# Kernel optimization log

Measured on AMD Instinct MI355X. Metric: run time of the kernel, lower is better.

Reference implementation:

```python
import jax, jax.numpy as jnp
import numpy as np

B, S, D, H = 4, 1024, 1024, 16
HD = D // H  # 64, even for RoPE


def _rope_tables(seq_len, head_dim):
    inv_freq = 1.0 / (10000.0 ** (jnp.arange(0, head_dim, 2, dtype=jnp.float32) / head_dim))
    pos = jnp.arange(seq_len, dtype=jnp.float32)
    ang = pos[:, None] * inv_freq[None, :]           # [S, HD/2]
    return jnp.cos(ang), jnp.sin(ang)


def _apply_rope(x, cos, sin):
    # x: [B, S, H, HD]; cos/sin: [S, HD/2] broadcast to [1, S, 1, HD/2]
    c = cos[None, :, None, :]
    s = sin[None, :, None, :]
    x1 = x[..., 0::2]
    x2 = x[..., 1::2]
    return jnp.concatenate([x1 * c - x2 * s, x1 * s + x2 * c], axis=-1)


def setup_inputs() -> dict:
    key = jax.random.key(0)
    ks = jax.random.split(key, 11)
    sc = 1.0 / np.sqrt(D)
    inp = {
        "query": jax.random.normal(ks[0], (B, S, D), jnp.float32),
        "key": jax.random.normal(ks[1], (B, S, D), jnp.float32),
        "value": jax.random.normal(ks[2], (B, S, D), jnp.float32),
        "mask": jnp.tril(jnp.ones((S, S), jnp.int32))[None, None],  # causal [1,1,S,S]
        "Wq": jax.random.normal(ks[3], (D, D), jnp.float32) * sc,
        "bq": jnp.zeros((D,), jnp.float32),
        "Wk": jax.random.normal(ks[4], (D, D), jnp.float32) * sc,
        "bk": jnp.zeros((D,), jnp.float32),
        "Wv": jax.random.normal(ks[5], (D, D), jnp.float32) * sc,
        "bv": jnp.zeros((D,), jnp.float32),
        "Wo": jax.random.normal(ks[6], (D, D), jnp.float32) * sc,
        "bo": jnp.zeros((D,), jnp.float32),
    }
    return inp


def reference(query, key, value, mask, Wq, bq, Wk, bk, Wv, bv, Wo, bo):
    Bq, Sq, _ = query.shape
    Sk = key.shape[1]
    q = (query @ Wq + bq).reshape(Bq, Sq, H, HD)
    k = (key @ Wk + bk).reshape(Bq, Sk, H, HD)
    v = (value @ Wv + bv).reshape(Bq, Sk, H, HD)
    cos, sin = _rope_tables(max(Sq, Sk), HD)
    q = _apply_rope(q, cos[:Sq], sin[:Sq])
    k = _apply_rope(k, cos[:Sk], sin[:Sk])
    scores = jnp.einsum("bqhd,bkhd->bhqk", q, k) / jnp.sqrt(jnp.float32(HD))
    scores = jnp.where(mask == 0, jnp.float32(-jnp.inf), scores)
    attn = jax.nn.softmax(scores, axis=-1)  # dropout p=0 (inference)
    ctx = jnp.einsum("bhqk,bkhd->bqhd", attn, v).reshape(Bq, Sq, D)
    return ctx @ Wo + bo
```

## Files before the change

kernel.cpp:

```cpp
#include <hip/hip_runtime.h>
#include <hip/hip_bf16.h>
#include <math.h>

#define B_DIM 4
#define S_DIM 1024
#define D_DIM 1024
#define H_DIM 16
#define HD_DIM 64
#define M_TOT 4096

typedef short short8 __attribute__((ext_vector_type(8)));
typedef float f32x4 __attribute__((ext_vector_type(4)));

__device__ inline float bf2f(short u)
{
    return __uint_as_float(((unsigned)(unsigned short)u) << 16);
}

__device__ inline void gload_lds16(const void* gsrc, void* lds)
{
    __builtin_amdgcn_global_load_lds(
        (const __attribute__((address_space(1))) unsigned int*)gsrc,
        (__attribute__((address_space(3))) unsigned int*)lds, 16, 0, 0);
}

__global__ __launch_bounds__(256) void preamble_kernel(
    const float* __restrict__ W0, const float* __restrict__ W1,
    const float* __restrict__ W2, const float* __restrict__ W3,
    __hip_bfloat16* __restrict__ T0, __hip_bfloat16* __restrict__ T1,
    __hip_bfloat16* __restrict__ T2, __hip_bfloat16* __restrict__ T3,
    float* __restrict__ tab)
{
    const int tid = threadIdx.x;
    if (blockIdx.z == 4) {
        const int fb = blockIdx.y * 32 + blockIdx.x;
        if (fb >= 128) return;
        const int t = fb * 256 + tid;
        const int pos = t >> 5, i = t & 31;
        float inv = powf(10000.0f, -(float)(2 * i) / 64.0f);
        float ang = (float)pos * inv;
        float s, c;
        sincosf(ang, &s, &c);
        tab[t] = c;
        tab[32768 + t] = s;
        return;
    }

    const float* W = (blockIdx.z == 0) ? W0 : (blockIdx.z == 1) ? W1
                    : (blockIdx.z == 2) ? W2 : W3;
    __hip_bfloat16* T = (blockIdx.z == 0) ? T0 : (blockIdx.z == 1) ? T1
                       : (blockIdx.z == 2) ? T2 : T3;

    __shared__ float tile[32][33];
    const int r = tid >> 3;
    const int c4 = (tid & 7) * 4;

    float4 v = *(const float4*)&W[(long)(blockIdx.y * 32 + r) * D_DIM + blockIdx.x * 32 + c4];
    tile[r][c4 + 0] = v.x;
    tile[r][c4 + 1] = v.y;
    tile[r][c4 + 2] = v.z;
    tile[r][c4 + 3] = v.w;
    __syncthreads();

    __hip_bfloat16 o[4];
    o[0] = __float2bfloat16(tile[c4 + 0][r]);
    o[1] = __float2bfloat16(tile[c4 + 1][r]);
    o[2] = __float2bfloat16(tile[c4 + 2][r]);
    o[3] = __float2bfloat16(tile[c4 + 3][r]);
    *(uint2*)&T[(long)(blockIdx.x * 32 + r) * D_DIM + blockIdx.y * 32 + c4] = *(uint2*)o;
}

__global__ __launch_bounds__(256, 3) void gemm_qkv_kernel(
    const float* __restrict__ Xq, const float* __restrict__ Xk,
    const float* __restrict__ Xv,
    const __hip_bfloat16* __restrict__ WtQ, const __hip_bfloat16* __restrict__ WtK,
    const __hip_bfloat16* __restrict__ WtV,
    const float* __restrict__ bq, const float* __restrict__ bk,
    const float* __restrict__ bv,
    __hip_bfloat16* __restrict__ Qo, __hip_bfloat16* __restrict__ Ko,
    __hip_bfloat16* __restrict__ Vto)
{
    __shared__ __align__(16) __hip_bfloat16 Al[2][128][40];
    __shared__ __align__(16) __hip_bfloat16 Bl[2][128][32];

    const int F = blockIdx.x + 8 * blockIdx.y + 256 * blockIdx.z;
    const int xcd = F & 7;
    const int sb = F >> 3;
    const int z = sb >> 5;
    const int n0 = (sb & 7) * 128;
    const int m0 = ((xcd << 2) | ((sb >> 3) & 3)) * 128;

    const float* X = (z == 0) ? Xq : (z == 1) ? Xk : Xv;
    const __hip_bfloat16* Wt = (z == 0) ? WtQ : (z == 1) ? WtK : WtV;
    const float* bias = (z == 0) ? bq : (z == 1) ? bk : bv;

    const int tid = threadIdx.x;
    const int l = tid & 63;
    const int w = tid >> 6;

    const int srow = w * 16 + (l >> 2);
    const int skc = (l & 3) * 8;
    const __hip_bfloat16* Bbase = Wt + (long)(n0 + srow) * D_DIM + skc;
    char* ldsB0 = (char*)&Bl[0][0][0] + w * 1024;
    char* ldsB1 = (char*)&Bl[1][0][0] + w * 1024;

    const int arow = tid >> 1;
    const int ak = (tid & 1) * 16;
    const float* Af = X + (long)(m0 + arow) * D_DIM + ak;

    const int lrow = l & 15;
    const int kg = l >> 4;
    const int wr = (w >> 1) * 64;
    const int wc = (w & 1) * 64;

    f32x4 acc[4][4];
#pragma unroll
    for (int i = 0; i < 4; ++i)
#pragma unroll
        for (int j = 0; j < 4; ++j) acc[i][j] = (f32x4){0.f, 0.f, 0.f, 0.f};

    float4 f0, f1, f2, f3;

    {
        f0 = *(const float4*)(Af);
        f1 = *(const float4*)(Af + 4);
        f2 = *(const float4*)(Af + 8);
        f3 = *(const float4*)(Af + 12);
        float fa[16] = {f0.x, f0.y, f0.z, f0.w, f1.x, f1.y, f1.z, f1.w,
                        f2.x, f2.y, f2.z, f2.w, f3.x, f3.y, f3.z, f3.w};
        __attribute__((aligned(16))) __hip_bfloat16 ab[16];
#pragma unroll
        for (int i = 0; i < 16; ++i) ab[i] = __float2bfloat16(fa[i]);
        *(short8*)&Al[0][arow][ak]     = ((const short8*)ab)[0];
        *(short8*)&Al[0][arow][ak + 8] = ((const short8*)ab)[1];
        gload_lds16(Bbase, ldsB0);
        gload_lds16(Bbase + 64 * D_DIM, ldsB0 + 4096);
        asm volatile("" ::: "memory");
        f0 = *(const float4*)(Af + 32);
        f1 = *(const float4*)(Af + 36);
        f2 = *(const float4*)(Af + 40);
        f3 = *(const float4*)(Af + 44);
        asm volatile("s_waitcnt vmcnt(4)" ::: "memory");
        asm volatile("s_waitcnt lgkmcnt(0)" ::: "memory");
        __builtin_amdgcn_s_barrier();
    }

    for (int t = 0; t < 32; ++t) {
        const int p = t & 1;
        const int q = p ^ 1;
        char* ldsBq = (q == 0) ? ldsB0 : ldsB1;

        if (t < 31) {
            const int k1 = (t + 1) * 32;
            gload_lds16(Bbase + k1, ldsBq);
            gload_lds16(Bbase + 64 * D_DIM + k1, ldsBq + 4096);
            float fa[16] = {f0.x, f0.y, f0.z, f0.w, f1.x, f1.y, f1.z, f1.w,
                            f2.x, f2.y, f2.z, f2.w, f3.x, f3.y, f3.z, f3.w};
            __attribute__((aligned(16))) __hip_bfloat16 ab[16];
#pragma unroll
            for (int i = 0; i < 16; ++i) ab[i] = __float2bfloat16(fa[i]);
            *(short8*)&Al[q][arow][ak]     = ((const short8*)ab)[0];
            *(short8*)&Al[q][arow][ak + 8] = ((const short8*)ab)[1];
        }
        asm volatile("" ::: "memory");
        if (t < 30) {
            const int k2 = (t + 2) * 32;
            f0 = *(const float4*)(Af + k2);
            f1 = *(const float4*)(Af + k2 + 4);
            f2 = *(const float4*)(Af + k2 + 8);
            f3 = *(const float4*)(Af + k2 + 12);
        }

        short8 af[4], bf[4];
#pragma unroll
        for (int i = 0; i < 4; ++i)
            af[i] = *(const short8*)&Al[p][wr + i * 16 + lrow][kg * 8];
#pragma unroll
        for (int j = 0; j < 4; ++j)
            bf[j] = *(const short8*)&Bl[p][wc + j * 16 + lrow][kg * 8];
#pragma unroll
        for (int i = 0; i < 4; ++i)
#pragma unroll
            for (int j = 0; j < 4; ++j)
                acc[i][j] = __builtin_amdgcn_mfma_f32_16x16x32_bf16(
                    af[i], bf[j], acc[i][j], 0, 0, 0);

        if (t < 31) {
            if (t < 30)
                asm volatile("s_waitcnt vmcnt(4)" ::: "memory");
            else
                asm volatile("s_waitcnt vmcnt(0)" ::: "memory");
            asm volatile("s_waitcnt lgkmcnt(0)" ::: "memory");
            __builtin_amdgcn_s_barrier();
        }
    }

#pragma unroll
    for (int i = 0; i < 4; ++i) {
#pragma unroll
        for (int j = 0; j < 4; ++j) {
            const int col = n0 + wc + j * 16 + lrow;
            const float bvs = bias[col];
            const int rbase = m0 + wr + i * 16 + kg * 4;
            if (z < 2) {
                __hip_bfloat16* Out = (z == 0) ? Qo : Ko;
#pragma unroll
                for (int r = 0; r < 4; ++r)
                    Out[(long)(rbase + r) * D_DIM + col] =
                        __float2bfloat16(acc[i][j][r] + bvs);
            } else {
                const int hh = col >> 6, dd = col & 63;
                const int bb = rbase >> 10, s0 = rbase & 1023;
                __hip_bfloat16 o[4];
#pragma unroll
                for (int r = 0; r < 4; ++r)
                    o[r] = __float2bfloat16(acc[i][j][r] + bvs);
                *(uint2*)&Vto[((long)((bb * H_DIM + hh) * HD_DIM + dd)) * S_DIM + s0] =
                    *(uint2*)o;
            }
        }
    }
}

__global__ __launch_bounds__(256, 2) void gemm_wo_kernel(
    const __hip_bfloat16* __restrict__ X, const __hip_bfloat16* __restrict__ Wt,
    const float* __restrict__ bias, float* __restrict__ Out)
{
    __shared__ __align__(16) __hip_bfloat16 Al[128][32];
    __shared__ __align__(16) __hip_bfloat16 Bl[64][32];

    const int F = blockIdx.x;
    const int xcd = F & 7;
    const int s = F >> 3;
    const int n0 = (s & 15) * 64;
    const int m0 = ((xcd << 2) | (s >> 4)) * 128;

    const int tid = threadIdx.x;
    const int l = tid & 63;
    const int w = tid >> 6;

    const int srow = w * 16 + (l >> 2);
    const int skc = (l & 3) * 8;
    const __hip_bfloat16* Abase = X + (long)(m0 + srow) * D_DIM + skc;
    const __hip_bfloat16* Bbase = Wt + (long)(n0 + srow) * D_DIM + skc;
    char* ldsA0 = (char*)&Al[0][0] + w * 1024;
    char* ldsB0 = (char*)&Bl[0][0] + w * 1024;

    const int lrow = l & 15;
    const int kg = l >> 4;
    const int wr = (w >> 1) * 64;
    const int wc = (w & 1) * 32;

    f32x4 acc[4][2];
#pragma unroll
    for (int i = 0; i < 4; ++i)
#pragma unroll
        for (int j = 0; j < 2; ++j) acc[i][j] = (f32x4){0.f, 0.f, 0.f, 0.f};

    for (int k0 = 0; k0 < D_DIM; k0 += 32) {
        __syncthreads();
        gload_lds16(Abase + k0, ldsA0);
        gload_lds16(Abase + 64 * D_DIM + k0, ldsA0 + 4096);
        gload_lds16(Bbase + k0, ldsB0);
        __syncthreads();

        short8 af[4], bf[2];
#pragma unroll
        for (int i = 0; i < 4; ++i)
            af[i] = *(const short8*)&Al[wr + i * 16 + lrow][kg * 8];
#pragma unroll
        for (int j = 0; j < 2; ++j)
            bf[j] = *(const short8*)&Bl[wc + j * 16 + lrow][kg * 8];
#pragma unroll
        for (int i = 0; i < 4; ++i)
#pragma unroll
            for (int j = 0; j < 2; ++j)
                acc[i][j] = __builtin_amdgcn_mfma_f32_16x16x32_bf16(
                    af[i], bf[j], acc[i][j], 0, 0, 0);
    }

#pragma unroll
    for (int i = 0; i < 4; ++i) {
#pragma unroll
        for (int j = 0; j < 2; ++j) {
            const int col = n0 + wc + j * 16 + lrow;
            const float bv = bias[col];
            const int rbase = m0 + wr + i * 16 + kg * 4;
#pragma unroll
            for (int r = 0; r < 4; ++r)
                Out[(long)(rbase + r) * D_DIM + col] = acc[i][j][r] + bv;
        }
    }
}

__global__ __launch_bounds__(256) void rope_bf16_kernel(
    const __hip_bfloat16* __restrict__ Qi, const __hip_bfloat16* __restrict__ Ki,
    __hip_bfloat16* __restrict__ Qo, __hip_bfloat16* __restrict__ Ko,
    const float* __restrict__ tab)
{
    const long t = (long)blockIdx.x * 256 + threadIdx.x;
    const int row = (int)(t >> 7);
    const int slot = (int)(t & 127);
    const int hh = slot >> 3;
    const int p0 = (slot & 7) * 4;
    const int pos = row & (S_DIM - 1);
    const bool isQ = (blockIdx.y == 0);
    const float scale = isQ ? 0.125f : 1.0f;

    const __hip_bfloat16* src = (isQ ? Qi : Ki) + (long)row * D_DIM + hh * HD_DIM;
    __hip_bfloat16* dst = (isQ ? Qo : Ko) + (long)row * D_DIM + hh * HD_DIM;

    short8 xv = *(const short8*)&src[2 * p0];
    float4 cv = *(const float4*)&tab[pos * 32 + p0];
    float4 sv = *(const float4*)&tab[32768 + pos * 32 + p0];
    float cc[4] = {cv.x, cv.y, cv.z, cv.w};
    float ss[4] = {sv.x, sv.y, sv.z, sv.w};

    __hip_bfloat16 o1[4], o2[4];
#pragma unroll
    for (int j = 0; j < 4; ++j) {
        float x1 = bf2f(xv[2 * j]);
        float x2 = bf2f(xv[2 * j + 1]);
        o1[j] = __float2bfloat16((x1 * cc[j] - x2 * ss[j]) * scale);
        o2[j] = __float2bfloat16((x1 * ss[j] + x2 * cc[j]) * scale);
    }
    *(uint2*)&dst[p0]      = *(uint2*)o1;
    *(uint2*)&dst[p0 + 32] = *(uint2*)o2;
}

#define KPAD 72

__global__ __launch_bounds__(256, 2) void attn_mfma_kernel(
    const __hip_bfloat16* __restrict__ Q,
    const __hip_bfloat16* __restrict__ K,
    const __hip_bfloat16* __restrict__ Vt,
    __hip_bfloat16* __restrict__ CTX)
{
    __shared__ __align__(16) __hip_bfloat16 Kl[64][KPAD];
    __shared__ __align__(16) __hip_bfloat16 Vl[64][KPAD];
    __shared__ __align__(16) __hip_bfloat16 Pl[4][32][KPAD];
    __shared__ __align__(16) float aS[4][2][16];

    const int tid = threadIdx.x;
    const int l = tid & 63;
    const int w = tid >> 6;

    const int bid = blockIdx.x + 8 * blockIdx.y + 128 * blockIdx.z;
    const int half = bid >> 8;
    const int idx = bid & 255;
    int qt = idx & 7;
    if (half) qt = 7 - qt;
    const int rest = idx >> 3;
    const int h = rest & 15;
    const int b = (rest >> 4) | (half << 1);

    const int lrow = l & 15;
    const int kg = l >> 4;
    const int kg4 = kg * 4;

    const int q0w = qt * 128 + w * 32;
    const long qrow_base = (long)b * S_DIM + q0w;

    short8 qf[2][2];
#pragma unroll
    for (int m = 0; m < 2; ++m)
#pragma unroll
        for (int ks = 0; ks < 2; ++ks)
            qf[m][ks] = *(const short8*)&Q[(qrow_base + m * 16 + lrow) * D_DIM +
                                           h * HD_DIM + ks * 32 + kg * 8];

    f32x4 ctx[2][4];
#pragma unroll
    for (int m = 0; m < 2; ++m)
#pragma unroll
        for (int d = 0; d < 4; ++d) ctx[m][d] = (f32x4){0.f, 0.f, 0.f, 0.f};
    float mrun[2] = {-1e30f, -1e30f};
    float lrun[2] = {0.f, 0.f};

    const int sr = tid >> 2;
    const int sc2 = (tid & 3) * 16;
    const __hip_bfloat16* Kg = K + ((long)b * S_DIM + sr) * D_DIM + h * HD_DIM + sc2;
    const __hip_bfloat16* Vg = Vt + ((long)((b * H_DIM + h) * HD_DIM) + sr) * S_DIM + sc2;

    const int ktmax = 2 * qt + 1;

    short8 kp0 = *(const short8*)Kg;
    short8 kp1 = *(const short8*)(Kg + 8);
    short8 vp0 = *(const short8*)Vg;
    short8 vp1 = *(const short8*)(Vg + 8);

    for (int kt = 0; kt <= ktmax; ++kt) {
        __syncthreads();
        *(short8*)&Kl[sr][sc2]     = kp0;
        *(short8*)&Kl[sr][sc2 + 8] = kp1;
        *(short8*)&Vl[sr][sc2]     = vp0;
        *(short8*)&Vl[sr][sc2 + 8] = vp1;
        if (kt < ktmax) {
            const __hip_bfloat16* kp = Kg + (long)(kt + 1) * 64 * D_DIM;
            const __hip_bfloat16* vp = Vg + (kt + 1) * 64;
            kp0 = *(const short8*)kp;
            kp1 = *(const short8*)(kp + 8);
            vp0 = *(const short8*)vp;
            vp1 = *(const short8*)(vp + 8);
        }
        __syncthreads();

        if (kt * 64 > q0w + 31) continue;

        f32x4 sac[2][4];
#pragma unroll
        for (int m = 0; m < 2; ++m)
#pragma unroll
            for (int nt = 0; nt < 4; ++nt) sac[m][nt] = (f32x4){0.f, 0.f, 0.f, 0.f};

        short8 kf[4][2];
#pragma unroll
        for (int nt = 0; nt < 4; ++nt)
#pragma unroll
            for (int ks = 0; ks < 2; ++ks)
                kf[nt][ks] = *(const short8*)&Kl[nt * 16 + lrow][ks * 32 + kg * 8];
#pragma unroll
        for (int m = 0; m < 2; ++m)
#pragma unroll
            for (int nt = 0; nt < 4; ++nt)
#pragma unroll
                for (int ks = 0; ks < 2; ++ks)
                    sac[m][nt] = __builtin_amdgcn_mfma_f32_16x16x32_bf16(
                        kf[nt][ks], qf[m][ks], sac[m][nt], 0, 0, 0);

        const bool partial = (kt * 64 + 63 > q0w);
        const int kbase = kt * 64;
#pragma unroll
        for (int m = 0; m < 2; ++m) {
            const int qg = q0w + m * 16 + lrow;
            float s[16];
#pragma unroll
            for (int nt = 0; nt < 4; ++nt)
#pragma unroll
                for (int r = 0; r < 4; ++r) {
                    float v = sac[m][nt][r];
                    if (partial && (kbase + nt * 16 + kg4 + r > qg)) v = -1e30f;
                    s[nt * 4 + r] = v;
                }
            float t8[8];
#pragma unroll
            for (int i = 0; i < 8; ++i) t8[i] = fmaxf(s[i], s[i + 8]);
#pragma unroll
            for (int i = 0; i < 4; ++i) t8[i] = fmaxf(t8[i], t8[i + 4]);
            float mx = fmaxf(fmaxf(t8[0], t8[1]), fmaxf(t8[2], t8[3]));
            mx = fmaxf(mx, __shfl_xor(mx, 16));
            mx = fmaxf(mx, __shfl_xor(mx, 32));
            const float mnew = fmaxf(mrun[m], mx);
            const float alpha = __expf(mrun[m] - mnew);
            mrun[m] = mnew;

            float p0s = 0.f, p1s = 0.f, p2s = 0.f, p3s = 0.f;
            __attribute__((aligned(8))) __hip_bfloat16 pb[16];
#pragma unroll
            for (int i = 0; i < 4; ++i) {
                float p = __expf(s[i] - mnew);      p0s += p; pb[i] = __float2bfloat16(p);
            }
#pragma unroll
            for (int i = 4; i < 8; ++i) {
                float p = __expf(s[i] - mnew);      p1s += p; pb[i] = __float2bfloat16(p);
            }
#pragma unroll
            for (int i = 8; i < 12; ++i) {
                float p = __expf(s[i] - mnew);      p2s += p; pb[i] = __float2bfloat16(p);
            }
#pragma unroll
            for (int i = 12; i < 16; ++i) {
                float p = __expf(s[i] - mnew);      p3s += p; pb[i] = __float2bfloat16(p);
            }
            float sum = (p0s + p1s) + (p2s + p3s);
            sum += __shfl_xor(sum, 16);
            sum += __shfl_xor(sum, 32);
            lrun[m] = lrun[m] * alpha + sum;

            if (kg == 0) aS[w][m][lrow] = alpha;
#pragma unroll
            for (int nt = 0; nt < 4; ++nt)
                *(uint2*)&Pl[w][m * 16 + lrow][nt * 16 + kg4] = *(uint2*)&pb[nt * 4];
        }

#pragma unroll
        for (int m = 0; m < 2; ++m) {
            f32x4 al4 = *(const f32x4*)&aS[w][m][kg4];
#pragma unroll
            for (int dt = 0; dt < 4; ++dt)
#pragma unroll
                for (int r = 0; r < 4; ++r) ctx[m][dt][r] *= al4[r];
        }

        short8 vf[4][2];
#pragma unroll
        for (int dt = 0; dt < 4; ++dt)
#pragma unroll
            for (int ks = 0; ks < 2; ++ks)
                vf[dt][ks] = *(const short8*)&Vl[dt * 16 + lrow][ks * 32 + kg * 8];
#pragma unroll
        for (int m = 0; m < 2; ++m) {
            short8 pf[2];
#pragma unroll
            for (int ks = 0; ks < 2; ++ks)
                pf[ks] = *(const short8*)&Pl[w][m * 16 + lrow][ks * 32 + kg * 8];
#pragma unroll
            for (int dt = 0; dt < 4; ++dt)
#pragma unroll
                for (int ks = 0; ks < 2; ++ks)
                    ctx[m][dt] = __builtin_amdgcn_mfma_f32_16x16x32_bf16(
                        pf[ks], vf[dt][ks], ctx[m][dt], 0, 0, 0);
        }
    }

    if (kg == 0) {
        aS[w][0][lrow] = lrun[0];
        aS[w][1][lrow] = lrun[1];
    }
#pragma unroll
    for (int m = 0; m < 2; ++m) {
        f32x4 lv = *(const f32x4*)&aS[w][m][kg4];
#pragma unroll
        for (int r = 0; r < 4; ++r) {
            const float inv_l = 1.0f / lv[r];
            const long rowoff = (qrow_base + m * 16 + kg4 + r) * D_DIM + h * HD_DIM;
#pragma unroll
            for (int dt = 0; dt < 4; ++dt)
                CTX[rowoff + dt * 16 + lrow] = __float2bfloat16(ctx[m][dt][r] * inv_l);
        }
    }
}

extern "C" void kernel_launch(void* const* d_in, const int* in_sizes, int n_in,
                              void* d_out, int out_size, void* d_ws, size_t ws_size,
                              hipStream_t stream)
{
    const float* query = (const float*)d_in[0];
    const float* key   = (const float*)d_in[1];
    const float* value = (const float*)d_in[2];
    const float* Wq = (const float*)d_in[4];
    const float* bq = (const float*)d_in[5];
    const float* Wk = (const float*)d_in[6];
    const float* bk = (const float*)d_in[7];
    const float* Wv = (const float*)d_in[8];
    const float* bv = (const float*)d_in[9];
    const float* Wo = (const float*)d_in[10];
    const float* bo = (const float*)d_in[11];

    char* wsb = (char*)d_ws;
    __hip_bfloat16* Qw    = (__hip_bfloat16*)(wsb);
    __hip_bfloat16* Kw    = (__hip_bfloat16*)(wsb + (8L  << 20));
    __hip_bfloat16* Vtb   = (__hip_bfloat16*)(wsb + (16L << 20));
    __hip_bfloat16* Qr    = (__hip_bfloat16*)(wsb + (24L << 20));
    __hip_bfloat16* Kr    = (__hip_bfloat16*)(wsb + (32L << 20));
    __hip_bfloat16* CTXbf = (__hip_bfloat16*)(wsb + (40L << 20));
    __hip_bfloat16* WtQ   = (__hip_bfloat16*)(wsb + (48L << 20));
    __hip_bfloat16* WtK   = (__hip_bfloat16*)(wsb + (50L << 20));
    __hip_bfloat16* WtV   = (__hip_bfloat16*)(wsb + (52L << 20));
    __hip_bfloat16* WtO   = (__hip_bfloat16*)(wsb + (54L << 20));
    float*          tab   = (float*)(wsb + (56L << 20));

    preamble_kernel<<<dim3(32, 32, 5), 256, 0, stream>>>(
        Wq, Wk, Wv, Wo, WtQ, WtK, WtV, WtO, tab);

    gemm_qkv_kernel<<<dim3(8, 32, 3), 256, 0, stream>>>(
        query, key, value, WtQ, WtK, WtV, bq, bk, bv, Qw, Kw, Vtb);

    rope_bf16_kernel<<<dim3(2048, 2), 256, 0, stream>>>(Qw, Kw, Qr, Kr, tab);

    attn_mfma_kernel<<<dim3(8, 16, 4), 256, 0, stream>>>(Qr, Kr, Vtb, CTXbf);

    gemm_wo_kernel<<<512, 256, 0, stream>>>(CTXbf, WtO, bo, (float*)d_out);
}
```

Before: 110.9 us.

## Triple-buffer weight tiles in QKV GEMM with prefetch distance two

The QKV projection GEMM moves from a double-buffered to a triple-buffered LDS ring for the weight (B) tiles, issuing async global-to-LDS loads two K-steps ahead. The K loop is manually unrolled by two, with a second register set for the fp32 activation prefetch, and the explicit vmcnt waits are dropped in favour of the compiler's waits on those registers. A sched_barrier places the fp32-to-bf16 conversion and LDS store of the next A tile after the MFMA block, aiming to hide global latency and overlap conversion with matrix math. The change costs 8 KB more LDS per block and more registers, which could reduce occupancy under the 3-blocks-per-CU launch bound. Correctness of the B tiles relies on in-order vmcnt retirement rather than explicit waits.

```diff
diff --git a/kernel.cpp b/kernel.cpp
--- a/kernel.cpp
+++ b/kernel.cpp
@@ -81,7 +81,7 @@
     __hip_bfloat16* __restrict__ Vto)
 {
     __shared__ __align__(16) __hip_bfloat16 Al[2][128][40];
-    __shared__ __align__(16) __hip_bfloat16 Bl[2][128][32];
+    __shared__ __align__(16) __hip_bfloat16 Bl[3][128][32];
 
     const int F = blockIdx.x + 8 * blockIdx.y + 256 * blockIdx.z;
     const int xcd = F & 7;
@@ -101,8 +101,7 @@
     const int srow = w * 16 + (l >> 2);
     const int skc = (l & 3) * 8;
     const __hip_bfloat16* Bbase = Wt + (long)(n0 + srow) * D_DIM + skc;
-    char* ldsB0 = (char*)&Bl[0][0][0] + w * 1024;
-    char* ldsB1 = (char*)&Bl[1][0][0] + w * 1024;
+    char* ldsBw = (char*)&Bl[0][0][0] + w * 1024;
 
     const int arow = tid >> 1;
     const int ak = (tid & 1) * 16;
@@ -120,6 +119,7 @@
         for (int j = 0; j < 4; ++j) acc[i][j] = (f32x4){0.f, 0.f, 0.f, 0.f};
 
     float4 f0, f1, f2, f3;
+    float4 g0, g1, g2, g3;
 
     {
         f0 = *(const float4*)(Af);
@@ -133,65 +133,108 @@
         for (int i = 0; i < 16; ++i) ab[i] = __float2bfloat16(fa[i]);
         *(short8*)&Al[0][arow][ak]     = ((const short8*)ab)[0];
         *(short8*)&Al[0][arow][ak + 8] = ((const short8*)ab)[1];
-        gload_lds16(Bbase, ldsB0);
-        gload_lds16(Bbase + 64 * D_DIM, ldsB0 + 4096);
+        gload_lds16(Bbase, ldsBw);
+        gload_lds16(Bbase + 64 * D_DIM, ldsBw + 4096);
+        gload_lds16(Bbase + 32, ldsBw + 8192);
+        gload_lds16(Bbase + 64 * D_DIM + 32, ldsBw + 8192 + 4096);
         asm volatile("" ::: "memory");
         f0 = *(const float4*)(Af + 32);
         f1 = *(const float4*)(Af + 36);
         f2 = *(const float4*)(Af + 40);
         f3 = *(const float4*)(Af + 44);
-        asm volatile("s_waitcnt vmcnt(4)" ::: "memory");
+        asm volatile("s_waitcnt vmcnt(6)" ::: "memory");
         asm volatile("s_waitcnt lgkmcnt(0)" ::: "memory");
         __builtin_amdgcn_s_barrier();
     }
 
-    for (int t = 0; t < 32; ++t) {
-        const int p = t & 1;
-        const int q = p ^ 1;
-        char* ldsBq = (q == 0) ? ldsB0 : ldsB1;
-
-        if (t < 31) {
-            const int k1 = (t + 1) * 32;
-            gload_lds16(Bbase + k1, ldsBq);
-            gload_lds16(Bbase + 64 * D_DIM + k1, ldsBq + 4096);
-            float fa[16] = {f0.x, f0.y, f0.z, f0.w, f1.x, f1.y, f1.z, f1.w,
-                            f2.x, f2.y, f2.z, f2.w, f3.x, f3.y, f3.z, f3.w};
-            __attribute__((aligned(16))) __hip_bfloat16 ab[16];
-#pragma unroll
-            for (int i = 0; i < 16; ++i) ab[i] = __float2bfloat16(fa[i]);
-            *(short8*)&Al[q][arow][ak]     = ((const short8*)ab)[0];
-            *(short8*)&Al[q][arow][ak + 8] = ((const short8*)ab)[1];
-        }
-        asm volatile("" ::: "memory");
-        if (t < 30) {
-            const int k2 = (t + 2) * 32;
-            f0 = *(const float4*)(Af + k2);
-            f1 = *(const float4*)(Af + k2 + 4);
-            f2 = *(const float4*)(Af + k2 + 8);
-            f3 = *(const float4*)(Af + k2 + 12);
-        }
-
-        short8 af[4], bf[4];
-#pragma unroll
-        for (int i = 0; i < 4; ++i)
-            af[i] = *(const short8*)&Al[p][wr + i * 16 + lrow][kg * 8];
-#pragma unroll
-        for (int j = 0; j < 4; ++j)
-            bf[j] = *(const short8*)&Bl[p][wc + j * 16 + lrow][kg * 8];
-#pragma unroll
-        for (int i = 0; i < 4; ++i)
+    int bc = 0;
+#pragma unroll 1
+    for (int tt = 0; tt < 16; ++tt) {
+        {
+            const int t = 2 * tt;
+            int bn = bc + 2; if (bn >= 3) bn -= 3;
+            if (tt < 15) {
+                const int k2 = (t + 2) * 32;
+                char* dst = ldsBw + bn * 8192;
+                gload_lds16(Bbase + k2, dst);
+                gload_lds16(Bbase + 64 * D_DIM + k2, dst + 4096);
+                asm volatile("" ::: "memory");
+                g0 = *(const float4*)(Af + k2);
+                g1 = *(const float4*)(Af + k2 + 4);
+                g2 = *(const float4*)(Af + k2 + 8);
+                g3 = *(const float4*)(Af + k2 + 12);
+            }
+            const __hip_bfloat16 (*Bc)[32] =
+                (const __hip_bfloat16(*)[32])((char*)&Bl[0][0][0] + bc * 8192);
+            short8 af[4], bf[4];
+#pragma unroll
+            for (int i = 0; i < 4; ++i)
+                af[i] = *(const short8*)&Al[0][wr + i * 16 + lrow][kg * 8];
 #pragma unroll
             for (int j = 0; j < 4; ++j)
-                acc[i][j] = __builtin_amdgcn_mfma_f32_16x16x32_bf16(
-                    af[i], bf[j], acc[i][j], 0, 0, 0);
-
-        if (t < 31) {
-            if (t < 30)
-                asm volatile("s_waitcnt vmcnt(4)" ::: "memory");
-            else
-                asm volatile("s_waitcnt vmcnt(0)" ::: "memory");
+                bf[j] = *(const short8*)&Bc[wc + j * 16 + lrow][kg * 8];
+#pragma unroll
+            for (int i = 0; i < 4; ++i)
+#pragma unroll
+                for (int j = 0; j < 4; ++j)
+                    acc[i][j] = __builtin_amdgcn_mfma_f32_16x16x32_bf16(
+                        af[i], bf[j], acc[i][j], 0, 0, 0);
+            __builtin_amdgcn_sched_barrier(0);
+            {
+                float fa[16] = {f0.x, f0.y, f0.z, f0.w, f1.x, f1.y, f1.z, f1.w,
+                                f2.x, f2.y, f2.z, f2.w, f3.x, f3.y, f3.z, f3.w};
+                __attribute__((aligned(16))) __hip_bfloat16 ab[16];
+#pragma unroll
+                for (int i = 0; i < 16; ++i) ab[i] = __float2bfloat16(fa[i]);
+                *(short8*)&Al[1][arow][ak]     = ((const short8*)ab)[0];
+                *(short8*)&Al[1][arow][ak + 8] = ((const short8*)ab)[1];
+            }
             asm volatile("s_waitcnt lgkmcnt(0)" ::: "memory");
             __builtin_amdgcn_s_barrier();
+            bc = bc + 1; if (bc >= 3) bc -= 3;
+        }
+        {
+            const int t = 2 * tt + 1;
+            int bn = bc + 2; if (bn >= 3) bn -= 3;
+            if (tt < 15) {
+                const int k2 = (t + 2) * 32;
+                char* dst = ldsBw + bn * 8192;
+                gload_lds16(Bbase + k2, dst);
+                gload_lds16(Bbase + 64 * D_DIM + k2, dst + 4096);
+                asm volatile("" ::: "memory");
+                f0 = *(const float4*)(Af + k2);
+                f1 = *(const float4*)(Af + k2 + 4);
+                f2 = *(const float4*)(Af + k2 + 8);
+                f3 = *(const float4*)(Af + k2 + 12);
+            }
+            const __hip_bfloat16 (*Bc)[32] =
+                (const __hip_bfloat16(*)[32])((char*)&Bl[0][0][0] + bc * 8192);
+            short8 af[4], bf[4];
+#pragma unroll
+            for (int i = 0; i < 4; ++i)
+                af[i] = *(const short8*)&Al[1][wr + i * 16 + lrow][kg * 8];
+#pragma unroll
+            for (int j = 0; j < 4; ++j)
+                bf[j] = *(const short8*)&Bc[wc + j * 16 + lrow][kg * 8];
+#pragma unroll
+            for (int i = 0; i < 4; ++i)
+#pragma unroll
+                for (int j = 0; j < 4; ++j)
+                    acc[i][j] = __builtin_amdgcn_mfma_f32_16x16x32_bf16(
+                        af[i], bf[j], acc[i][j], 0, 0, 0);
+            if (tt < 15) {
+                __builtin_amdgcn_sched_barrier(0);
+                float fa[16] = {g0.x, g0.y, g0.z, g0.w, g1.x, g1.y, g1.z, g1.w,
+                                g2.x, g2.y, g2.z, g2.w, g3.x, g3.y, g3.z, g3.w};
+                __attribute__((aligned(16))) __hip_bfloat16 ab[16];
+#pragma unroll
+                for (int i = 0; i < 16; ++i) ab[i] = __float2bfloat16(fa[i]);
+                *(short8*)&Al[0][arow][ak]     = ((const short8*)ab)[0];
+                *(short8*)&Al[0][arow][ak + 8] = ((const short8*)ab)[1];
+                asm volatile("s_waitcnt lgkmcnt(0)" ::: "memory");
+                __builtin_amdgcn_s_barrier();
+            }
+            bc = bc + 1; if (bc >= 3) bc -= 3;
         }
     }
 
```

New measurement: 112.6 us. Within noise of the previous version (+1.5%).
